# Kernel tuning notes

Measured on AMD Instinct MI355X. Metric: run time of the kernel, lower is better.

## Reference

```python
import jax, jax.numpy as jnp
import numpy as np

B, T, C, H = 2, 2048, 768, 12
HD = C // H


def setup_inputs() -> dict:
    key = jax.random.key(0)
    ks = jax.random.split(key, 8)
    s = 0.02
    return {
        "x": jax.random.normal(ks[0], (B, T, C), dtype=jnp.float32),
        "attn_mask1": jax.random.randint(ks[1], (B, T), 0, 2, dtype=jnp.int32),
        "Wq": jax.random.normal(ks[2], (C, C), dtype=jnp.float32) * s,
        "bq": jnp.zeros((C,), dtype=jnp.float32),
        "Wk": jax.random.normal(ks[3], (C, C), dtype=jnp.float32) * s,
        "bk": jnp.zeros((C,), dtype=jnp.float32),
        "Wv": jax.random.normal(ks[4], (C, C), dtype=jnp.float32) * s,
        "bv": jnp.zeros((C,), dtype=jnp.float32),
        "Wp": jax.random.normal(ks[5], (C, C), dtype=jnp.float32) * s,
        "bp": jnp.zeros((C,), dtype=jnp.float32),
    }


def reference(x, attn_mask1, Wq, bq, Wk, bk, Wv, bv, Wp, bp):
    b, t, c = x.shape
    # linear projections, split heads -> [B, H, T, HD]
    def heads(w, bias):
        return (x @ w.T + bias).reshape(b, t, H, HD).transpose(0, 2, 1, 3)
    q = heads(Wq, bq)
    k = heads(Wk, bk)
    v = heads(Wv, bv)
    scale = 1.0 / jnp.sqrt(jnp.asarray(HD, dtype=x.dtype))
    att = jnp.einsum("bhqd,bhkd->bhqk", q, k) * scale  # [B,H,T,T]
    # key-padding mask: original tiles [B,T] along the query axis only
    key_mask = (attn_mask1 == 0)[:, None, None, :]  # [B,1,1,T]
    att = jnp.where(key_mask, -jnp.inf, att)
    att = jax.nn.softmax(att, axis=-1)
    y = jnp.einsum("bhqk,bhkd->bhqd", att, v)  # [B,H,T,HD]
    y = y.transpose(0, 2, 1, 3).reshape(b, t, c)
    return y @ Wp.T + bp
```

## Files before the change

kernel.cpp:

```cpp
#include <hip/hip_runtime.h>
#include <stdint.h>

typedef unsigned short u16;
typedef __bf16 bf16x8 __attribute__((ext_vector_type(8)));
typedef float f32x4 __attribute__((ext_vector_type(4)));

#define BB 2
#define TT 2048
#define CC 768
#define HH 12
#define HD 64
#define MTOT (BB*TT)
#define N_QKV (3*CC)

__device__ __forceinline__ u16 f2bf(float f) {
    uint32_t u = __builtin_bit_cast(uint32_t, f);
    u = (u + 0x7fffu + ((u >> 16) & 1u)) >> 16;
    return (u16)u;
}
__device__ __forceinline__ float bf2f(u16 h) {
    return __builtin_bit_cast(float, (uint32_t)h << 16);
}

union U16x8 { uint4 v; u16 s[8]; };

__device__ __forceinline__ void gl_lds16(const u16* g, u16* l) {
    __builtin_amdgcn_global_load_lds(
        (const __attribute__((address_space(1))) uint32_t*)g,
        (__attribute__((address_space(3))) uint32_t*)l, 16, 0, 0);
}

__global__ void k_cvt(const float* __restrict__ src, u16* __restrict__ dst, int n4) {
    int i = blockIdx.x * blockDim.x + threadIdx.x;
    if (i >= n4) return;
    float4 v = reinterpret_cast<const float4*>(src)[i];
    uint lo = (uint)f2bf(v.x) | ((uint)f2bf(v.y) << 16);
    uint hi = (uint)f2bf(v.z) | ((uint)f2bf(v.w) << 16);
    reinterpret_cast<uint2*>(dst)[i] = make_uint2(lo, hi);
}

__global__ void k_mask(const int* __restrict__ m, float* __restrict__ o, int n) {
    int i = blockIdx.x * blockDim.x + threadIdx.x;
    if (i < n) o[i] = (m[i] == 0) ? -1e30f : 0.0f;
}

__global__ void k_packb(const float* __restrict__ bq, const float* __restrict__ bk,
                        const float* __restrict__ bv, float* __restrict__ o) {
    int i = blockIdx.x * blockDim.x + threadIdx.x;
    if (i < CC) o[i] = bq[i];
    else if (i < 2 * CC) o[i] = bk[i - CC];
    else if (i < 3 * CC) o[i] = bv[i - 2 * CC];
}

#define GBM 128
#define GBN 128
#define GBK 32

__global__ __launch_bounds__(256)
void k_gemm(const u16* __restrict__ A, const u16* __restrict__ W,
            const float* __restrict__ bias, int K, int N, int mode,
            u16* __restrict__ outQ, u16* __restrict__ outK, u16* __restrict__ outVt,
            float* __restrict__ outLin)
{
    __shared__ alignas(16) u16 As[GBM][GBK];
    __shared__ alignas(16) u16 Bs[GBN][GBK];

    const int tid  = threadIdx.x;
    const int lane = tid & 63;
    const int wave = tid >> 6;
    const int m0 = blockIdx.y * GBM;
    const int n0 = blockIdx.x * GBN;
    const int wm = (wave >> 1) * 64;
    const int wn = (wave & 1) * 64;

    f32x4 acc[4][4];
#pragma unroll
    for (int m = 0; m < 4; ++m)
#pragma unroll
        for (int n = 0; n < 4; ++n)
            acc[m][n] = f32x4{0.f, 0.f, 0.f, 0.f};

    const int lrow = lane >> 2;
    const int lcol = (lane & 3) * 8;

    for (int k0 = 0; k0 < K; k0 += GBK) {
        __syncthreads();
        {
            const int r0 = wave * 32;
            gl_lds16(A + (size_t)(m0 + r0 + lrow) * K + k0 + lcol,      &As[r0][0]);
            gl_lds16(A + (size_t)(m0 + r0 + 16 + lrow) * K + k0 + lcol, &As[r0 + 16][0]);
            gl_lds16(W + (size_t)(n0 + r0 + lrow) * K + k0 + lcol,      &Bs[r0][0]);
            gl_lds16(W + (size_t)(n0 + r0 + 16 + lrow) * K + k0 + lcol, &Bs[r0 + 16][0]);
        }
        __syncthreads();

        bf16x8 af[4], bfb[4];
#pragma unroll
        for (int m = 0; m < 4; ++m)
            af[m] = *reinterpret_cast<const bf16x8*>(&As[wm + m * 16 + (lane & 15)][(lane >> 4) * 8]);
#pragma unroll
        for (int n = 0; n < 4; ++n)
            bfb[n] = *reinterpret_cast<const bf16x8*>(&Bs[wn + n * 16 + (lane & 15)][(lane >> 4) * 8]);
#pragma unroll
        for (int m = 0; m < 4; ++m)
#pragma unroll
            for (int n = 0; n < 4; ++n)
                acc[m][n] = __builtin_amdgcn_mfma_f32_16x16x32_bf16(af[m], bfb[n], acc[m][n], 0, 0, 0);
    }

    const int col   = lane & 15;
    const int rbase = (lane >> 4) * 4;
#pragma unroll
    for (int m = 0; m < 4; ++m) {
#pragma unroll
        for (int n = 0; n < 4; ++n) {
            const int gn = n0 + wn + n * 16 + col;
            const float bv = bias[gn];
#pragma unroll
            for (int j = 0; j < 4; ++j) {
                const int gm = m0 + wm + m * 16 + rbase + j;
                const float val = acc[m][n][j] + bv;
                if (mode == 1) {
                    outLin[(size_t)gm * N + gn] = val;
                } else {
                    const int proj = gn / CC;
                    const int c = gn - proj * CC;
                    const int h = c >> 6, hd = c & 63;
                    const int b = gm >> 11, t = gm & (TT - 1);
                    if (proj == 0)
                        outQ[((size_t)(b * HH + h) * TT + t) * HD + hd] = f2bf(val);
                    else if (proj == 1)
                        outK[((size_t)(b * HH + h) * TT + t) * HD + hd] = f2bf(val);
                    else
                        outVt[((size_t)(b * HH + h) * HD + hd) * TT + t] = f2bf(val);
                }
            }
        }
    }
}

__global__ __launch_bounds__(64)
void k_attn(const u16* __restrict__ Qh, const u16* __restrict__ Kh,
            const u16* __restrict__ Vt, const float* __restrict__ maskb,
            u16* __restrict__ Y)
{
    __shared__ alignas(16) u16 Ps[32][136];

    const int lane = threadIdx.x;
    const int raw  = blockIdx.x;
    const int virt = (raw & 7) * 192 + (raw >> 3);
    const int bh = virt >> 6;
    const int b  = bh / HH, h = bh % HH;
    const int q0 = (virt & 63) * 32;

    const u16* Qp = Qh + (size_t)bh * TT * HD;
    const u16* Kp = Kh + (size_t)bh * TT * HD;
    const u16* Vp = Vt + (size_t)bh * HD * TT;
    const float* mrow = maskb + b * TT;

    const int l15 = lane & 15;
    const int lg  = lane >> 4;

    bf16x8 qf[2][2];
#pragma unroll
    for (int m = 0; m < 2; ++m)
#pragma unroll
        for (int ks = 0; ks < 2; ++ks) {
            U16x8 t;
            t.v = *reinterpret_cast<const uint4*>(
                Qp + (size_t)(q0 + m * 16 + l15) * HD + ks * 32 + lg * 8);
            U16x8 o;
#pragma unroll
            for (int j = 0; j < 8; ++j) o.s[j] = f2bf(bf2f(t.s[j]) * 0.125f);
            qf[m][ks] = __builtin_bit_cast(bf16x8, o.v);
        }

    f32x4 oacc[2][4];
#pragma unroll
    for (int m = 0; m < 2; ++m)
#pragma unroll
        for (int n = 0; n < 4; ++n) oacc[m][n] = f32x4{0.f, 0.f, 0.f, 0.f};
    float mrun[2][4], lrun[2][4];
#pragma unroll
    for (int m = 0; m < 2; ++m)
#pragma unroll
        for (int j = 0; j < 4; ++j) { mrun[m][j] = -1e30f; lrun[m][j] = 0.f; }

    for (int kt = 0; kt < TT; kt += 128) {
        f32x4 sacc[2][8];
#pragma unroll
        for (int m = 0; m < 2; ++m)
#pragma unroll
            for (int n = 0; n < 8; ++n) sacc[m][n] = f32x4{0.f, 0.f, 0.f, 0.f};
#pragma unroll
        for (int ks = 0; ks < 2; ++ks) {
            uint4 kfr[8];
#pragma unroll
            for (int n = 0; n < 8; ++n)
                kfr[n] = *reinterpret_cast<const uint4*>(
                    Kp + (size_t)(kt + n * 16 + l15) * HD + ks * 32 + lg * 8);
#pragma unroll
            for (int n = 0; n < 8; ++n) {
                bf16x8 kf = __builtin_bit_cast(bf16x8, kfr[n]);
#pragma unroll
                for (int m = 0; m < 2; ++m)
                    sacc[m][n] = __builtin_amdgcn_mfma_f32_16x16x32_bf16(qf[m][ks], kf, sacc[m][n], 0, 0, 0);
            }
        }

        float mbv[8];
#pragma unroll
        for (int n = 0; n < 8; ++n) mbv[n] = mrow[kt + n * 16 + l15];

        float tmax[2][4];
#pragma unroll
        for (int m = 0; m < 2; ++m)
#pragma unroll
            for (int j = 0; j < 4; ++j) tmax[m][j] = -1e30f;
#pragma unroll
        for (int m = 0; m < 2; ++m)
#pragma unroll
            for (int n = 0; n < 8; ++n)
#pragma unroll
                for (int j = 0; j < 4; ++j) {
                    float s = sacc[m][n][j] + mbv[n];
                    sacc[m][n][j] = s;
                    tmax[m][j] = fmaxf(tmax[m][j], s);
                }
#pragma unroll
        for (int off = 1; off < 16; off <<= 1)
#pragma unroll
            for (int m = 0; m < 2; ++m)
#pragma unroll
                for (int j = 0; j < 4; ++j)
                    tmax[m][j] = fmaxf(tmax[m][j], __shfl_xor(tmax[m][j], off));

        float scl[2][4];
#pragma unroll
        for (int m = 0; m < 2; ++m)
#pragma unroll
            for (int j = 0; j < 4; ++j) {
                float mnew = fmaxf(mrun[m][j], tmax[m][j]);
                scl[m][j] = __expf(mrun[m][j] - mnew);
                mrun[m][j] = mnew;
            }

        float rs[2][4];
#pragma unroll
        for (int m = 0; m < 2; ++m)
#pragma unroll
            for (int j = 0; j < 4; ++j) rs[m][j] = 0.f;
#pragma unroll
        for (int m = 0; m < 2; ++m)
#pragma unroll
            for (int n = 0; n < 8; ++n)
#pragma unroll
                for (int j = 0; j < 4; ++j) {
                    float s = sacc[m][n][j];
                    float p = (s < -1e29f) ? 0.f : __expf(s - mrun[m][j]);
                    sacc[m][n][j] = p;
                    rs[m][j] += p;
                }
#pragma unroll
        for (int off = 1; off < 16; off <<= 1)
#pragma unroll
            for (int m = 0; m < 2; ++m)
#pragma unroll
                for (int j = 0; j < 4; ++j) rs[m][j] += __shfl_xor(rs[m][j], off);
#pragma unroll
        for (int m = 0; m < 2; ++m)
#pragma unroll
            for (int j = 0; j < 4; ++j) lrun[m][j] = lrun[m][j] * scl[m][j] + rs[m][j];

#pragma unroll
        for (int m = 0; m < 2; ++m)
#pragma unroll
            for (int n = 0; n < 8; ++n)
#pragma unroll
                for (int j = 0; j < 4; ++j)
                    Ps[m * 16 + lg * 4 + j][n * 16 + l15] = f2bf(sacc[m][n][j]);

#pragma unroll
        for (int m = 0; m < 2; ++m)
#pragma unroll
            for (int n = 0; n < 4; ++n)
#pragma unroll
                for (int j = 0; j < 4; ++j) oacc[m][n][j] *= scl[m][j];

#pragma unroll
        for (int ks2 = 0; ks2 < 4; ++ks2) {
            bf16x8 pf[2];
#pragma unroll
            for (int m = 0; m < 2; ++m)
                pf[m] = *reinterpret_cast<const bf16x8*>(&Ps[m * 16 + l15][ks2 * 32 + lg * 8]);
            uint4 vfr[4];
#pragma unroll
            for (int n = 0; n < 4; ++n)
                vfr[n] = *reinterpret_cast<const uint4*>(
                    Vp + (size_t)(n * 16 + l15) * TT + kt + ks2 * 32 + lg * 8);
#pragma unroll
            for (int n = 0; n < 4; ++n) {
                bf16x8 vf = __builtin_bit_cast(bf16x8, vfr[n]);
#pragma unroll
                for (int m = 0; m < 2; ++m)
                    oacc[m][n] = __builtin_amdgcn_mfma_f32_16x16x32_bf16(pf[m], vf, oacc[m][n], 0, 0, 0);
            }
        }
    }

#pragma unroll
    for (int m = 0; m < 2; ++m)
#pragma unroll
        for (int n = 0; n < 4; ++n)
#pragma unroll
            for (int j = 0; j < 4; ++j) {
                const int t = q0 + m * 16 + lg * 4 + j;
                const int c = h * 64 + n * 16 + l15;
                Y[((size_t)b * TT + t) * CC + c] = f2bf(oacc[m][n][j] / lrun[m][j]);
            }
}

extern "C" void kernel_launch(void* const* d_in, const int* in_sizes, int n_in,
                              void* d_out, int out_size, void* d_ws, size_t ws_size,
                              hipStream_t stream)
{
    const float* x    = (const float*)d_in[0];
    const int*   mask = (const int*)d_in[1];
    const float* Wq   = (const float*)d_in[2];
    const float* bq   = (const float*)d_in[3];
    const float* Wk   = (const float*)d_in[4];
    const float* bk   = (const float*)d_in[5];
    const float* Wv   = (const float*)d_in[6];
    const float* bv   = (const float*)d_in[7];
    const float* Wp   = (const float*)d_in[8];
    const float* bp   = (const float*)d_in[9];
    float* out = (float*)d_out;

    char* w = (char*)d_ws;
    auto alloc = [&](size_t bytes) {
        char* p = w;
        w += (bytes + 255) & ~(size_t)255;
        return p;
    };
    u16* x_bf    = (u16*)alloc((size_t)MTOT * CC * 2);
    u16* wqkv_bf = (u16*)alloc((size_t)3 * CC * CC * 2);
    u16* wp_bf   = (u16*)alloc((size_t)CC * CC * 2);
    u16* qh      = (u16*)alloc((size_t)MTOT * CC * 2);
    u16* kh      = (u16*)alloc((size_t)MTOT * CC * 2);
    u16* vt      = (u16*)alloc((size_t)MTOT * CC * 2);
    u16* y_bf    = (u16*)alloc((size_t)MTOT * CC * 2);
    float* maskb = (float*)alloc((size_t)BB * TT * 4);
    float* bqkv  = (float*)alloc((size_t)N_QKV * 4);

    const int NX4 = MTOT * CC / 4;
    k_cvt<<<(NX4 + 255) / 256, 256, 0, stream>>>(x, x_bf, NX4);
    const int NW4 = CC * CC / 4;
    k_cvt<<<(NW4 + 255) / 256, 256, 0, stream>>>(Wq, wqkv_bf, NW4);
    k_cvt<<<(NW4 + 255) / 256, 256, 0, stream>>>(Wk, wqkv_bf + (size_t)CC * CC, NW4);
    k_cvt<<<(NW4 + 255) / 256, 256, 0, stream>>>(Wv, wqkv_bf + (size_t)2 * CC * CC, NW4);
    k_cvt<<<(NW4 + 255) / 256, 256, 0, stream>>>(Wp, wp_bf, NW4);
    k_mask<<<(BB * TT + 255) / 256, 256, 0, stream>>>(mask, maskb, BB * TT);
    k_packb<<<(N_QKV + 255) / 256, 256, 0, stream>>>(bq, bk, bv, bqkv);

    k_gemm<<<dim3(N_QKV / GBN, MTOT / GBM), 256, 0, stream>>>(
        x_bf, wqkv_bf, bqkv, CC, N_QKV, 0, qh, kh, vt, nullptr);

    k_attn<<<dim3(1536), 64, 0, stream>>>(qh, kh, vt, maskb, y_bf);

    k_gemm<<<dim3(CC / GBN, MTOT / GBM), 256, 0, stream>>>(
        y_bf, wp_bf, bp, CC, CC, 1, nullptr, nullptr, nullptr, out);
}
```

Measured before the change: 268.4 us.

## Split attention keys across two blocks and merge partials in combine kernel

Splits each query tile's key range into two halves handled by separate single-wave blocks, doubling the grid. Each block writes unnormalized fp32 output plus running max and sum, and a new combine kernel merges them with log-sum-exp weights and writes the bf16 attention output. The aim is more parallelism and occupancy for the 64-thread attention kernel. The cost is an extra launch and fp32 partial traffic to and from memory. It also drops the masked-score guard in the exp, relying on exp underflow, which risks NaN or a wrong sum if a half has every key masked.

```diff
diff --git a/kernel.cpp b/kernel.cpp
--- a/kernel.cpp
+++ b/kernel.cpp
@@ -12,6 +12,8 @@
 #define HD 64
 #define MTOT (BB*TT)
 #define N_QKV (3*CC)
+#define NSPLIT 2
+#define NROWS (BB*HH*TT)
 
 __device__ __forceinline__ u16 f2bf(float f) {
     uint32_t u = __builtin_bit_cast(uint32_t, f);
@@ -142,20 +144,23 @@
 __global__ __launch_bounds__(64)
 void k_attn(const u16* __restrict__ Qh, const u16* __restrict__ Kh,
             const u16* __restrict__ Vt, const float* __restrict__ maskb,
-            u16* __restrict__ Y)
+            float* __restrict__ Opart, float* __restrict__ Mpart, float* __restrict__ Lpart)
 {
     __shared__ alignas(16) u16 Ps[32][136];
 
     const int lane = threadIdx.x;
     const int raw  = blockIdx.x;
-    const int virt = (raw & 7) * 192 + (raw >> 3);
-    const int bh = virt >> 6;
-    const int b  = bh / HH, h = bh % HH;
-    const int q0 = (virt & 63) * 32;
+    const int virt = (raw & 7) * 384 + (raw >> 3);
+    const int bh  = virt >> 7;
+    const int rem = virt & 127;
+    const int q0  = (rem >> 1) * 32;
+    const int sp  = rem & 1;
+    const int kt0 = sp * (TT / NSPLIT);
 
     const u16* Qp = Qh + (size_t)bh * TT * HD;
     const u16* Kp = Kh + (size_t)bh * TT * HD;
     const u16* Vp = Vt + (size_t)bh * HD * TT;
+    const int b = bh / HH;
     const float* mrow = maskb + b * TT;
 
     const int l15 = lane & 15;
@@ -186,7 +191,7 @@
 #pragma unroll
         for (int j = 0; j < 4; ++j) { mrun[m][j] = -1e30f; lrun[m][j] = 0.f; }
 
-    for (int kt = 0; kt < TT; kt += 128) {
+    for (int kt = kt0; kt < kt0 + TT / NSPLIT; kt += 128) {
         f32x4 sacc[2][8];
 #pragma unroll
         for (int m = 0; m < 2; ++m)
@@ -256,8 +261,7 @@
             for (int n = 0; n < 8; ++n)
 #pragma unroll
                 for (int j = 0; j < 4; ++j) {
-                    float s = sacc[m][n][j];
-                    float p = (s < -1e29f) ? 0.f : __expf(s - mrun[m][j]);
+                    float p = __expf(sacc[m][n][j] - mrun[m][j]);
                     sacc[m][n][j] = p;
                     rs[m][j] += p;
                 }
@@ -308,16 +312,44 @@
         }
     }
 
+    const size_t rbase_ = (size_t)sp * NROWS + (size_t)bh * TT;
 #pragma unroll
     for (int m = 0; m < 2; ++m)
 #pragma unroll
         for (int n = 0; n < 4; ++n)
 #pragma unroll
             for (int j = 0; j < 4; ++j) {
-                const int t = q0 + m * 16 + lg * 4 + j;
-                const int c = h * 64 + n * 16 + l15;
-                Y[((size_t)b * TT + t) * CC + c] = f2bf(oacc[m][n][j] / lrun[m][j]);
-            }
+                const size_t r = rbase_ + q0 + m * 16 + lg * 4 + j;
+                Opart[r * HD + n * 16 + l15] = oacc[m][n][j];
+            }
+    if (l15 == 0) {
+#pragma unroll
+        for (int m = 0; m < 2; ++m)
+#pragma unroll
+            for (int j = 0; j < 4; ++j) {
+                const size_t r = rbase_ + q0 + m * 16 + lg * 4 + j;
+                Mpart[r] = mrun[m][j];
+                Lpart[r] = lrun[m][j];
+            }
+    }
+}
+
+__global__ __launch_bounds__(256)
+void k_comb(const float* __restrict__ Opart, const float* __restrict__ Mpart,
+            const float* __restrict__ Lpart, u16* __restrict__ Y)
+{
+    const int wave = threadIdx.x >> 6;
+    const int d    = threadIdx.x & 63;
+    const size_t r = (size_t)blockIdx.x * 4 + wave;
+    const float m1 = Mpart[r],         l1 = Lpart[r];
+    const float m2 = Mpart[NROWS + r], l2 = Lpart[NROWS + r];
+    const float mm = fmaxf(m1, m2);
+    const float w1 = __expf(m1 - mm), w2 = __expf(m2 - mm);
+    const float l  = l1 * w1 + l2 * w2;
+    const float o  = Opart[r * HD + d] * w1 + Opart[((size_t)NROWS + r) * HD + d] * w2;
+    const int bh = (int)(r >> 11), t = (int)(r & (TT - 1));
+    const int b = bh / HH, h = bh % HH;
+    Y[((size_t)b * TT + t) * CC + h * 64 + d] = f2bf(o / l);
 }
 
 extern "C" void kernel_launch(void* const* d_in, const int* in_sizes, int n_in,
@@ -351,6 +383,9 @@
     u16* y_bf    = (u16*)alloc((size_t)MTOT * CC * 2);
     float* maskb = (float*)alloc((size_t)BB * TT * 4);
     float* bqkv  = (float*)alloc((size_t)N_QKV * 4);
+    float* Opart = (float*)alloc((size_t)NSPLIT * NROWS * HD * 4);
+    float* Mpart = (float*)alloc((size_t)NSPLIT * NROWS * 4);
+    float* Lpart = (float*)alloc((size_t)NSPLIT * NROWS * 4);
 
     const int NX4 = MTOT * CC / 4;
     k_cvt<<<(NX4 + 255) / 256, 256, 0, stream>>>(x, x_bf, NX4);
@@ -365,7 +400,8 @@
     k_gemm<<<dim3(N_QKV / GBN, MTOT / GBM), 256, 0, stream>>>(
         x_bf, wqkv_bf, bqkv, CC, N_QKV, 0, qh, kh, vt, nullptr);
 
-    k_attn<<<dim3(1536), 64, 0, stream>>>(qh, kh, vt, maskb, y_bf);
+    k_attn<<<dim3(1536 * NSPLIT), 64, 0, stream>>>(qh, kh, vt, maskb, Opart, Mpart, Lpart);
+    k_comb<<<dim3(NROWS / 4), 256, 0, stream>>>(Opart, Mpart, Lpart, y_bf);
 
     k_gemm<<<dim3(CC / GBN, MTOT / GBM), 256, 0, stream>>>(
         y_bf, wp_bf, bp, CC, CC, 1, nullptr, nullptr, nullptr, out);
```

Result: slower. 284.2 us (+5.9%).
